# Optimization experiments

Measured on AMD Instinct MI355X. Metric: run time of the kernel, lower is better.

## Reference

```python
import jax, jax.numpy as jnp
import numpy as np

NUM_HEADS = 32
HIDDEN = 4096
HEAD_DIM = HIDDEN // NUM_HEADS
BATCH = 1
SEQ = 2048


def setup_inputs() -> dict:
    key = jax.random.key(0)
    ks = jax.random.split(key, 8)
    hidden_states = jax.random.normal(ks[0], (BATCH, SEQ, HIDDEN), dtype=jnp.float32)
    residual = jax.random.normal(ks[1], (BATCH, SEQ, HIDDEN), dtype=jnp.float32)
    # BLOOM alibi: [batch*heads, 1, kv_len], broadcast over q_length in baddbmm
    alibi = jax.random.normal(ks[2], (BATCH * NUM_HEADS, 1, SEQ), dtype=jnp.float32) * 0.1
    # causal boolean mask: True = masked (filled with -inf before softmax)
    attention_mask = ~jnp.tril(jnp.ones((SEQ, SEQ), dtype=bool))[None, None, :, :]
    scale = 0.02
    Wqkv = jax.random.normal(ks[3], (3 * HIDDEN, HIDDEN), dtype=jnp.float32) * scale
    bqkv = jax.random.normal(ks[4], (3 * HIDDEN,), dtype=jnp.float32) * scale
    Wd = jax.random.normal(ks[5], (HIDDEN, HIDDEN), dtype=jnp.float32) * scale
    bd = jax.random.normal(ks[6], (HIDDEN,), dtype=jnp.float32) * scale
    return {"hidden_states": hidden_states, "residual": residual, "alibi": alibi,
            "attention_mask": attention_mask, "Wqkv": Wqkv, "bqkv": bqkv,
            "Wd": Wd, "bd": bd}


def reference(hidden_states, residual, alibi, attention_mask, Wqkv, bqkv, Wd, bd):
    B, S, H = hidden_states.shape
    nh, hd = NUM_HEADS, HEAD_DIM
    inv_norm = 1.0 / np.sqrt(hd).astype(np.float32)

    # fused QKV projection, BLOOM interleaved layout [B, S, nh, 3, hd]
    fused = hidden_states @ Wqkv.T + bqkv           # [B, S, 3H]
    fused = fused.reshape(B, S, nh, 3, hd)
    q = jnp.transpose(fused[..., 0, :], (0, 2, 1, 3))  # [B, nh, S, hd]
    k = jnp.transpose(fused[..., 1, :], (0, 2, 1, 3))  # [B, nh, S, hd]
    v = jnp.transpose(fused[..., 2, :], (0, 2, 1, 3))  # [B, nh, S, hd]

    # baddbmm: alibi + inv_norm * Q @ K^T
    alibi_b = alibi.reshape(B, nh, 1, S)                # broadcast over q_length
    scores = alibi_b + inv_norm * jnp.einsum('bhqd,bhkd->bhqk', q, k)
    scores = jnp.where(attention_mask, jnp.finfo(scores.dtype).min, scores)
    probs = jax.nn.softmax(scores, axis=-1)             # [B, nh, S, S]

    ctx = jnp.einsum('bhqk,bhkd->bhqd', probs, v)       # [B, nh, S, hd]
    ctx = jnp.transpose(ctx, (0, 2, 1, 3)).reshape(B, S, H)
    out = ctx @ Wd.T + bd
    return residual + out
```

## Files before the change

kernel.cpp:

```cpp
#include <hip/hip_runtime.h>


#define SEQL 2048
#define HIDN 4096
#define NHEAD 32
#define HDIM 128
#define H3 12288

typedef __bf16 bf16x8 __attribute__((ext_vector_type(8)));
typedef float f32x4 __attribute__((ext_vector_type(4)));
typedef unsigned short u16x8 __attribute__((ext_vector_type(8)));

__device__ __forceinline__ unsigned short f2bf(float f) {
  union { float f; unsigned u; } v; v.f = f;
  return (unsigned short)((v.u + 0x7FFFu + ((v.u >> 16) & 1u)) >> 16);
}

__device__ __forceinline__ void gload_lds16(const void* g, void* l) {
  __builtin_amdgcn_global_load_lds(
      (const __attribute__((address_space(1))) void*)g,
      (__attribute__((address_space(3))) void*)l, 16, 0, 0);
}

__global__ __launch_bounds__(256) void cvt_f32_bf16(
    const float* __restrict__ in, unsigned short* __restrict__ out, long long n) {
  long long i = ((long long)blockIdx.x * blockDim.x + threadIdx.x) * 8;
  long long stride = (long long)gridDim.x * blockDim.x * 8;
  for (; i < n; i += stride) {
    float4 a = *(const float4*)(in + i);
    float4 b = *(const float4*)(in + i + 4);
    u16x8 o;
    o[0] = f2bf(a.x); o[1] = f2bf(a.y); o[2] = f2bf(a.z); o[3] = f2bf(a.w);
    o[4] = f2bf(b.x); o[5] = f2bf(b.y); o[6] = f2bf(b.z); o[7] = f2bf(b.w);
    *(u16x8*)(out + i) = o;
  }
}

template <int EPI>
__global__ __launch_bounds__(256) void gemm_nt(
    const unsigned short* __restrict__ A, const unsigned short* __restrict__ B,
    int M, int N, int K,
    const float* __restrict__ bias, const float* __restrict__ residual,
    float* __restrict__ outf,
    unsigned short* __restrict__ q_bf, unsigned short* __restrict__ k_bf,
    unsigned short* __restrict__ v_t) {
  __shared__ unsigned short As[128 * 64];
  __shared__ unsigned short Bs[128 * 64];

  const int tid = threadIdx.x;
  const int l = tid & 63;
  const int w = tid >> 6;
  const int wr = (w >> 1) * 64;
  const int wc = (w & 1) * 64;

  const int nb = gridDim.x;
  const int lin = (blockIdx.x & 7) * (nb >> 3) + (blockIdx.x >> 3);
  const int tm0 = (lin & 15) * 128;
  const int tn0 = (lin >> 4) * 128;

  const int lr = l >> 3;
  const int lc = (l & 7) ^ lr;

  f32x4 acc[4][4] = {};

  for (int kt = 0; kt < K; kt += 64) {
    __syncthreads();
#pragma unroll
    for (int i = 0; i < 4; ++i) {
      const int row = w * 32 + i * 8 + lr;
      gload_lds16(&A[(long long)(tm0 + row) * K + kt + lc * 8],
                  (char*)As + (w * 4 + i) * 1024);
      gload_lds16(&B[(long long)(tn0 + row) * K + kt + lc * 8],
                  (char*)Bs + (w * 4 + i) * 1024);
    }
    __syncthreads();
#pragma unroll
    for (int kk = 0; kk < 2; ++kk) {
      const int colb = kk * 64 + (l >> 4) * 16;
      bf16x8 af[4], bfr[4];
#pragma unroll
      for (int m = 0; m < 4; ++m) {
        int row = wr + m * 16 + (l & 15);
        af[m] = *(const bf16x8*)((char*)As + row * 128 + (colb ^ ((row & 7) << 4)));
      }
#pragma unroll
      for (int n = 0; n < 4; ++n) {
        int row = wc + n * 16 + (l & 15);
        bfr[n] = *(const bf16x8*)((char*)Bs + row * 128 + (colb ^ ((row & 7) << 4)));
      }
#pragma unroll
      for (int m = 0; m < 4; ++m)
#pragma unroll
        for (int n = 0; n < 4; ++n)
          acc[m][n] = __builtin_amdgcn_mfma_f32_16x16x32_bf16(af[m], bfr[n], acc[m][n], 0, 0, 0);
    }
  }

#pragma unroll
  for (int m = 0; m < 4; ++m) {
#pragma unroll
    for (int n = 0; n < 4; ++n) {
      const int col = tn0 + wc + n * 16 + (l & 15);
      const float bv = bias[col];
#pragma unroll
      for (int r = 0; r < 4; ++r) {
        const int rowg = tm0 + wr + m * 16 + (l >> 4) * 4 + r;
        float v = acc[m][n][r] + bv;
        if (EPI == 0) {
          const int head = col / 384;
          const int rem = col - head * 384;
          const int which = rem >> 7;
          const int d = rem & 127;
          const unsigned short bv16 = f2bf(v);
          if (which == 0)
            q_bf[(long long)(head * SEQL + rowg) * HDIM + d] = bv16;
          else if (which == 1)
            k_bf[(long long)(head * SEQL + rowg) * HDIM + d] = bv16;
          else
            v_t[(long long)(head * HDIM + d) * SEQL + rowg] = bv16;
        } else {
          const long long idx = (long long)rowg * N + col;
          outf[idx] = v + residual[idx];
        }
      }
    }
  }
}

__global__ __launch_bounds__(256) void attn_fwd(
    const unsigned short* __restrict__ q_bf, const unsigned short* __restrict__ k_bf,
    const unsigned short* __restrict__ v_t, const float* __restrict__ alibi,
    unsigned short* __restrict__ ctx_bf) {
  __shared__ unsigned short Ks[64 * 128];
  __shared__ unsigned short Vs[128 * 64];
  __shared__ unsigned short Ps[4][16 * 64];
  __shared__ float Al[SEQL];

  const int tid = threadIdx.x;
  const int l = tid & 63;
  const int w = tid >> 6;

  const float LOG2E = 1.4426950408889634f;

  const int b = blockIdx.x;
  const int i_ = b >> 3;
  const int h = (b & 7) * 4 + (i_ & 3);
  const int qtile = 31 - (i_ >> 2);
  const int qw = qtile * 64 + w * 16;

  for (int i = tid; i < SEQL; i += 256) Al[i] = alibi[h * SEQL + i] * LOG2E;

  bf16x8 qf[4];
  {
    const unsigned short* qp =
        &q_bf[(long long)(h * SEQL + qw + (l & 15)) * HDIM + (l >> 4) * 8];
#pragma unroll
    for (int kk = 0; kk < 4; ++kk) qf[kk] = *(const bf16x8*)(qp + kk * 32);
  }

  f32x4 oacc[8] = {};
  float mrun[4] = {-__builtin_inff(), -__builtin_inff(), -__builtin_inff(), -__builtin_inff()};
  float lrun[4] = {0.f, 0.f, 0.f, 0.f};
  const float inv_norm2 = 0.08838834764831845f * 1.4426950408889634f;

  const int kR = l >> 4, kC = l & 15;
  const int vR = l >> 3, vC = (l & 7) ^ vR;

  const int ntiles = qtile + 1;
  for (int t = 0; t < ntiles; ++t) {
    const int kv0 = t * 64;
    __syncthreads();
#pragma unroll
    for (int i = 0; i < 4; ++i) {
      const int krow = w * 16 + i * 4 + kR;
      const int ksrc = kC ^ ((i & 1) * 4 + kR);
      gload_lds16(&k_bf[(long long)(h * SEQL + kv0 + krow) * HDIM + ksrc * 8],
                  (char*)Ks + (w * 4 + i) * 1024);
      const int vrow = w * 32 + i * 8 + vR;
      gload_lds16(&v_t[(long long)(h * HDIM + vrow) * SEQL + kv0 + vC * 8],
                  (char*)Vs + (w * 4 + i) * 1024);
    }
    __syncthreads();

    f32x4 sacc[4] = {};
#pragma unroll
    for (int kk = 0; kk < 4; ++kk) {
      const int colb = kk * 64 + (l >> 4) * 16;
#pragma unroll
      for (int n = 0; n < 4; ++n) {
        int row = n * 16 + (l & 15);
        bf16x8 kf = *(const bf16x8*)((char*)Ks + row * 256 + (colb ^ ((row & 7) << 4)));
        sacc[n] = __builtin_amdgcn_mfma_f32_16x16x32_bf16(qf[kk], kf, sacc[n], 0, 0, 0);
      }
    }

    float sc[4][4];
#pragma unroll
    for (int n = 0; n < 4; ++n) {
      const int kv = kv0 + n * 16 + (l & 15);
      const float al = Al[kv];
#pragma unroll
      for (int r = 0; r < 4; ++r) {
        const int qrow = qw + (l >> 4) * 4 + r;
        float v = al + inv_norm2 * sacc[n][r];
        sc[n][r] = (kv > qrow) ? -__builtin_inff() : v;
      }
    }

#pragma unroll
    for (int r = 0; r < 4; ++r) {
      float m0 = fmaxf(fmaxf(sc[0][r], sc[1][r]), fmaxf(sc[2][r], sc[3][r]));
      m0 = fmaxf(m0, __shfl_xor(m0, 1, 64));
      m0 = fmaxf(m0, __shfl_xor(m0, 2, 64));
      m0 = fmaxf(m0, __shfl_xor(m0, 4, 64));
      m0 = fmaxf(m0, __shfl_xor(m0, 8, 64));
      if (__ballot(m0 > mrun[r] + 11.0f)) {
        const float mnew = fmaxf(mrun[r], m0);
        const float scale = exp2f(mrun[r] - mnew);
        mrun[r] = mnew;
        lrun[r] *= scale;
#pragma unroll
        for (int n2 = 0; n2 < 8; ++n2) oacc[n2][r] *= scale;
      }
      float p0 = 0.f;
#pragma unroll
      for (int n = 0; n < 4; ++n) {
        const float pv = exp2f(sc[n][r] - mrun[r]);
        sc[n][r] = pv;
        p0 += pv;
      }
      p0 += __shfl_xor(p0, 1, 64);
      p0 += __shfl_xor(p0, 2, 64);
      p0 += __shfl_xor(p0, 4, 64);
      p0 += __shfl_xor(p0, 8, 64);
      lrun[r] += p0;
    }

#pragma unroll
    for (int n = 0; n < 4; ++n)
#pragma unroll
      for (int r = 0; r < 4; ++r) {
        const int row = (l >> 4) * 4 + r;
        const int colp = n * 16 + (l & 15);
        *(unsigned short*)((char*)Ps[w] + row * 128 + ((colp * 2) ^ ((row & 7) << 4))) =
            f2bf(sc[n][r]);
      }
    __threadfence_block();
    bf16x8 pf[2];
#pragma unroll
    for (int kk2 = 0; kk2 < 2; ++kk2) {
      const int row = l & 15;
      const int colb = kk2 * 64 + (l >> 4) * 16;
      pf[kk2] = *(const bf16x8*)((char*)Ps[w] + row * 128 + (colb ^ ((row & 7) << 4)));
    }

#pragma unroll
    for (int n2 = 0; n2 < 8; ++n2) {
#pragma unroll
      for (int kk2 = 0; kk2 < 2; ++kk2) {
        const int row = n2 * 16 + (l & 15);
        const int colb = kk2 * 64 + (l >> 4) * 16;
        bf16x8 vf = *(const bf16x8*)((char*)Vs + row * 128 + (colb ^ ((row & 7) << 4)));
        oacc[n2] = __builtin_amdgcn_mfma_f32_16x16x32_bf16(pf[kk2], vf, oacc[n2], 0, 0, 0);
      }
    }
  }

#pragma unroll
  for (int n2 = 0; n2 < 8; ++n2)
#pragma unroll
    for (int r = 0; r < 4; ++r) {
      const int qrow = qw + (l >> 4) * 4 + r;
      const int col = h * HDIM + n2 * 16 + (l & 15);
      ctx_bf[(long long)qrow * HIDN + col] = f2bf(oacc[n2][r] / lrun[r]);
    }
}

extern "C" void kernel_launch(void* const* d_in, const int* in_sizes, int n_in,
                              void* d_out, int out_size, void* d_ws, size_t ws_size,
                              hipStream_t stream) {
  const float* hidden = (const float*)d_in[0];
  const float* residual = (const float*)d_in[1];
  const float* alibi = (const float*)d_in[2];
  const float* Wqkv = (const float*)d_in[4];
  const float* bqkv = (const float*)d_in[5];
  const float* Wd = (const float*)d_in[6];
  const float* bd = (const float*)d_in[7];
  float* out = (float*)d_out;

  char* ws = (char*)d_ws;
  const size_t MB16 = 16777216;
  unsigned short* q_bf = (unsigned short*)(ws);
  unsigned short* k_bf = (unsigned short*)(ws + MB16);
  unsigned short* v_t = (unsigned short*)(ws + 2 * MB16);
  unsigned short* hid_bf = (unsigned short*)(ws + 3 * MB16);
  unsigned short* wqkv_bf = (unsigned short*)(ws + 4 * MB16);
  unsigned short* wd_bf = (unsigned short*)(ws + 4 * MB16);
  unsigned short* ctx_bf = (unsigned short*)(ws + 4 * MB16 + 33554432);

  cvt_f32_bf16<<<4096, 256, 0, stream>>>(hidden, hid_bf, (long long)SEQL * HIDN);
  cvt_f32_bf16<<<24576, 256, 0, stream>>>(Wqkv, wqkv_bf, (long long)H3 * HIDN);

  gemm_nt<0><<<(SEQL / 128) * (H3 / 128), 256, 0, stream>>>(
      hid_bf, wqkv_bf, SEQL, H3, HIDN, bqkv, nullptr, nullptr, q_bf, k_bf, v_t);

  cvt_f32_bf16<<<8192, 256, 0, stream>>>(Wd, wd_bf, (long long)HIDN * HIDN);

  attn_fwd<<<NHEAD * (SEQL / 64), 256, 0, stream>>>(q_bf, k_bf, v_t, alibi, ctx_bf);

  gemm_nt<1><<<(SEQL / 128) * (HIDN / 128), 256, 0, stream>>>(
      ctx_bf, wd_bf, SEQL, HIDN, HIDN, bd, residual, out, nullptr, nullptr, nullptr);
}
```

Baseline: 503.4 us.

## Double-buffer K/V tiles in attention with async prefetch and wave-level causal skip

The attention kernel now double-buffers K and V tiles in LDS. The next tile is issued with global_load_lds before computing the current one, and explicit vmcnt waits plus raw barriers replace the two __syncthreads per iteration. Waves whose 16 query rows lie entirely before the KV tile skip the score/softmax/PV work, and the alibi preload is limited to the needed length. This doubles K/V LDS use (about 64KB plus alibi), which may reduce occupancy, and relies on hand-counted vmcnt values being correct.

```diff
diff --git a/kernel.cpp b/kernel.cpp
--- a/kernel.cpp
+++ b/kernel.cpp
@@ -21,6 +21,14 @@
       (const __attribute__((address_space(1))) void*)g,
       (__attribute__((address_space(3))) void*)l, 16, 0, 0);
 }
+
+#define BARX()                                  \
+  do {                                          \
+    __builtin_amdgcn_sched_barrier(0);          \
+    __builtin_amdgcn_s_barrier();               \
+    __builtin_amdgcn_sched_barrier(0);          \
+  } while (0)
+#define VMW(n) asm volatile("s_waitcnt vmcnt(" #n ")" ::: "memory")
 
 __global__ __launch_bounds__(256) void cvt_f32_bf16(
     const float* __restrict__ in, unsigned short* __restrict__ out, long long n) {
@@ -131,8 +139,8 @@
     const unsigned short* __restrict__ q_bf, const unsigned short* __restrict__ k_bf,
     const unsigned short* __restrict__ v_t, const float* __restrict__ alibi,
     unsigned short* __restrict__ ctx_bf) {
-  __shared__ unsigned short Ks[64 * 128];
-  __shared__ unsigned short Vs[128 * 64];
+  __shared__ unsigned short Ks[2][64 * 128];
+  __shared__ unsigned short Vs[2][128 * 64];
   __shared__ unsigned short Ps[4][16 * 64];
   __shared__ float Al[SEQL];
 
@@ -147,8 +155,11 @@
   const int h = (b & 7) * 4 + (i_ & 3);
   const int qtile = 31 - (i_ >> 2);
   const int qw = qtile * 64 + w * 16;
-
-  for (int i = tid; i < SEQL; i += 256) Al[i] = alibi[h * SEQL + i] * LOG2E;
+  const int ntiles = qtile + 1;
+
+  const int alN = ntiles * 64;
+  for (int i = tid; i < alN; i += 256) Al[i] = alibi[h * SEQL + i] * LOG2E;
+  asm volatile("s_waitcnt lgkmcnt(0)" ::: "memory");
 
   bf16x8 qf[4];
   {
@@ -166,104 +177,118 @@
   const int kR = l >> 4, kC = l & 15;
   const int vR = l >> 3, vC = (l & 7) ^ vR;
 
-  const int ntiles = qtile + 1;
-  for (int t = 0; t < ntiles; ++t) {
+  auto stage = [&](int t) {
+    const int buf = t & 1;
     const int kv0 = t * 64;
-    __syncthreads();
 #pragma unroll
     for (int i = 0; i < 4; ++i) {
-      const int krow = w * 16 + i * 4 + kR;
+      const int c = w * 4 + i;
+      const int krow = c * 4 + kR;
       const int ksrc = kC ^ ((i & 1) * 4 + kR);
       gload_lds16(&k_bf[(long long)(h * SEQL + kv0 + krow) * HDIM + ksrc * 8],
-                  (char*)Ks + (w * 4 + i) * 1024);
-      const int vrow = w * 32 + i * 8 + vR;
+                  (char*)Ks[buf] + c * 1024);
+      const int vrow = c * 8 + vR;
       gload_lds16(&v_t[(long long)(h * HDIM + vrow) * SEQL + kv0 + vC * 8],
-                  (char*)Vs + (w * 4 + i) * 1024);
-    }
-    __syncthreads();
-
-    f32x4 sacc[4] = {};
-#pragma unroll
-    for (int kk = 0; kk < 4; ++kk) {
-      const int colb = kk * 64 + (l >> 4) * 16;
+                  (char*)Vs[buf] + c * 1024);
+    }
+  };
+
+  stage(0);
+  for (int t = 0; t < ntiles; ++t) {
+    const int cur = t & 1;
+    const int kv0 = t * 64;
+    const bool g = (t + 1) < ntiles;
+    if (g) stage(t + 1);
+    if (g) { VMW(8); } else { VMW(0); }
+    BARX();
+
+    if (kv0 <= qw + 15) {
+      f32x4 sacc[4] = {};
+#pragma unroll
+      for (int kk = 0; kk < 4; ++kk) {
+        const int colb = kk * 64 + (l >> 4) * 16;
+#pragma unroll
+        for (int n = 0; n < 4; ++n) {
+          int row = n * 16 + (l & 15);
+          bf16x8 kf = *(const bf16x8*)((char*)Ks[cur] + row * 256 +
+                                       (colb ^ ((row & 7) << 4)));
+          sacc[n] = __builtin_amdgcn_mfma_f32_16x16x32_bf16(qf[kk], kf, sacc[n], 0, 0, 0);
+        }
+      }
+
+      float sc[4][4];
 #pragma unroll
       for (int n = 0; n < 4; ++n) {
-        int row = n * 16 + (l & 15);
-        bf16x8 kf = *(const bf16x8*)((char*)Ks + row * 256 + (colb ^ ((row & 7) << 4)));
-        sacc[n] = __builtin_amdgcn_mfma_f32_16x16x32_bf16(qf[kk], kf, sacc[n], 0, 0, 0);
-      }
-    }
-
-    float sc[4][4];
-#pragma unroll
-    for (int n = 0; n < 4; ++n) {
-      const int kv = kv0 + n * 16 + (l & 15);
-      const float al = Al[kv];
+        const int kv = kv0 + n * 16 + (l & 15);
+        const float al = Al[kv];
+#pragma unroll
+        for (int r = 0; r < 4; ++r) {
+          const int qrow = qw + (l >> 4) * 4 + r;
+          float v = al + inv_norm2 * sacc[n][r];
+          sc[n][r] = (kv > qrow) ? -__builtin_inff() : v;
+        }
+      }
+
 #pragma unroll
       for (int r = 0; r < 4; ++r) {
-        const int qrow = qw + (l >> 4) * 4 + r;
-        float v = al + inv_norm2 * sacc[n][r];
-        sc[n][r] = (kv > qrow) ? -__builtin_inff() : v;
-      }
-    }
-
-#pragma unroll
-    for (int r = 0; r < 4; ++r) {
-      float m0 = fmaxf(fmaxf(sc[0][r], sc[1][r]), fmaxf(sc[2][r], sc[3][r]));
-      m0 = fmaxf(m0, __shfl_xor(m0, 1, 64));
-      m0 = fmaxf(m0, __shfl_xor(m0, 2, 64));
-      m0 = fmaxf(m0, __shfl_xor(m0, 4, 64));
-      m0 = fmaxf(m0, __shfl_xor(m0, 8, 64));
-      if (__ballot(m0 > mrun[r] + 11.0f)) {
-        const float mnew = fmaxf(mrun[r], m0);
-        const float scale = exp2f(mrun[r] - mnew);
-        mrun[r] = mnew;
-        lrun[r] *= scale;
-#pragma unroll
-        for (int n2 = 0; n2 < 8; ++n2) oacc[n2][r] *= scale;
-      }
-      float p0 = 0.f;
-#pragma unroll
-      for (int n = 0; n < 4; ++n) {
-        const float pv = exp2f(sc[n][r] - mrun[r]);
-        sc[n][r] = pv;
-        p0 += pv;
-      }
-      p0 += __shfl_xor(p0, 1, 64);
-      p0 += __shfl_xor(p0, 2, 64);
-      p0 += __shfl_xor(p0, 4, 64);
-      p0 += __shfl_xor(p0, 8, 64);
-      lrun[r] += p0;
-    }
-
-#pragma unroll
-    for (int n = 0; n < 4; ++n)
-#pragma unroll
-      for (int r = 0; r < 4; ++r) {
-        const int row = (l >> 4) * 4 + r;
-        const int colp = n * 16 + (l & 15);
-        *(unsigned short*)((char*)Ps[w] + row * 128 + ((colp * 2) ^ ((row & 7) << 4))) =
-            f2bf(sc[n][r]);
-      }
-    __threadfence_block();
-    bf16x8 pf[2];
-#pragma unroll
-    for (int kk2 = 0; kk2 < 2; ++kk2) {
-      const int row = l & 15;
-      const int colb = kk2 * 64 + (l >> 4) * 16;
-      pf[kk2] = *(const bf16x8*)((char*)Ps[w] + row * 128 + (colb ^ ((row & 7) << 4)));
-    }
-
-#pragma unroll
-    for (int n2 = 0; n2 < 8; ++n2) {
+        float m0 = fmaxf(fmaxf(sc[0][r], sc[1][r]), fmaxf(sc[2][r], sc[3][r]));
+        m0 = fmaxf(m0, __shfl_xor(m0, 1, 64));
+        m0 = fmaxf(m0, __shfl_xor(m0, 2, 64));
+        m0 = fmaxf(m0, __shfl_xor(m0, 4, 64));
+        m0 = fmaxf(m0, __shfl_xor(m0, 8, 64));
+        if (__ballot(m0 > mrun[r] + 11.0f)) {
+          const float mnew = fmaxf(mrun[r], m0);
+          const float scale = exp2f(mrun[r] - mnew);
+          mrun[r] = mnew;
+          lrun[r] *= scale;
+#pragma unroll
+          for (int n2 = 0; n2 < 8; ++n2) oacc[n2][r] *= scale;
+        }
+        float p0 = 0.f;
+#pragma unroll
+        for (int n = 0; n < 4; ++n) {
+          const float pv = exp2f(sc[n][r] - mrun[r]);
+          sc[n][r] = pv;
+          p0 += pv;
+        }
+        p0 += __shfl_xor(p0, 1, 64);
+        p0 += __shfl_xor(p0, 2, 64);
+        p0 += __shfl_xor(p0, 4, 64);
+        p0 += __shfl_xor(p0, 8, 64);
+        lrun[r] += p0;
+      }
+
+#pragma unroll
+      for (int n = 0; n < 4; ++n)
+#pragma unroll
+        for (int r = 0; r < 4; ++r) {
+          const int row = (l >> 4) * 4 + r;
+          const int colp = n * 16 + (l & 15);
+          *(unsigned short*)((char*)Ps[w] + row * 128 + ((colp * 2) ^ ((row & 7) << 4))) =
+              f2bf(sc[n][r]);
+        }
+      __threadfence_block();
+      bf16x8 pf[2];
 #pragma unroll
       for (int kk2 = 0; kk2 < 2; ++kk2) {
-        const int row = n2 * 16 + (l & 15);
+        const int row = l & 15;
         const int colb = kk2 * 64 + (l >> 4) * 16;
-        bf16x8 vf = *(const bf16x8*)((char*)Vs + row * 128 + (colb ^ ((row & 7) << 4)));
-        oacc[n2] = __builtin_amdgcn_mfma_f32_16x16x32_bf16(pf[kk2], vf, oacc[n2], 0, 0, 0);
-      }
-    }
+        pf[kk2] = *(const bf16x8*)((char*)Ps[w] + row * 128 + (colb ^ ((row & 7) << 4)));
+      }
+
+#pragma unroll
+      for (int n2 = 0; n2 < 8; ++n2) {
+#pragma unroll
+        for (int kk2 = 0; kk2 < 2; ++kk2) {
+          const int row = n2 * 16 + (l & 15);
+          const int colb = kk2 * 64 + (l >> 4) * 16;
+          bf16x8 vf = *(const bf16x8*)((char*)Vs[cur] + row * 128 +
+                                       (colb ^ ((row & 7) << 4)));
+          oacc[n2] = __builtin_amdgcn_mfma_f32_16x16x32_bf16(pf[kk2], vf, oacc[n2], 0, 0, 0);
+        }
+      }
+    }
+    BARX();
   }
 
 #pragma unroll
```

Measured after the change: 506.8 us. About the same (+0.7%).

## Process 128 query rows per attention block, two 16-row groups per wave

Applied to the files above, without the earlier changes.

The attention kernel now gives each block a 128-row query tile, with each wave handling 32 rows as two 16-row MFMA groups. Each K/V tile loaded into LDS is reused across twice as many queries, which halves global K/V traffic and the per-tile barrier overhead. Waves skip KV tiles that lie fully above their causal diagonal. The cost is more registers for the doubled accumulators, and there are half as many blocks (512), which may lower occupancy and load balance across CUs.

```diff
diff --git a/kernel.cpp b/kernel.cpp
--- a/kernel.cpp
+++ b/kernel.cpp
@@ -133,7 +133,7 @@
     unsigned short* __restrict__ ctx_bf) {
   __shared__ unsigned short Ks[64 * 128];
   __shared__ unsigned short Vs[128 * 64];
-  __shared__ unsigned short Ps[4][16 * 64];
+  __shared__ unsigned short Ps[4][32 * 64];
   __shared__ float Al[SEQL];
 
   const int tid = threadIdx.x;
@@ -145,135 +145,154 @@
   const int b = blockIdx.x;
   const int i_ = b >> 3;
   const int h = (b & 7) * 4 + (i_ & 3);
-  const int qtile = 31 - (i_ >> 2);
-  const int qw = qtile * 64 + w * 16;
-
-  for (int i = tid; i < SEQL; i += 256) Al[i] = alibi[h * SEQL + i] * LOG2E;
-
-  bf16x8 qf[4];
-  {
+  const int qtile = 15 - (i_ >> 2);
+  const int qw = qtile * 128 + w * 32;
+  const int ntiles = 2 * qtile + 2;
+
+  for (int i = tid; i < ntiles * 64; i += 256) Al[i] = alibi[h * SEQL + i] * LOG2E;
+
+  bf16x8 qf[2][4];
+#pragma unroll
+  for (int g = 0; g < 2; ++g) {
     const unsigned short* qp =
-        &q_bf[(long long)(h * SEQL + qw + (l & 15)) * HDIM + (l >> 4) * 8];
-#pragma unroll
-    for (int kk = 0; kk < 4; ++kk) qf[kk] = *(const bf16x8*)(qp + kk * 32);
-  }
-
-  f32x4 oacc[8] = {};
-  float mrun[4] = {-__builtin_inff(), -__builtin_inff(), -__builtin_inff(), -__builtin_inff()};
-  float lrun[4] = {0.f, 0.f, 0.f, 0.f};
+        &q_bf[(long long)(h * SEQL + qw + g * 16 + (l & 15)) * HDIM + (l >> 4) * 8];
+#pragma unroll
+    for (int kk = 0; kk < 4; ++kk) qf[g][kk] = *(const bf16x8*)(qp + kk * 32);
+  }
+
+  f32x4 oacc[2][8] = {};
+  float mrun[2][4], lrun[2][4];
+#pragma unroll
+  for (int g = 0; g < 2; ++g)
+#pragma unroll
+    for (int r = 0; r < 4; ++r) { mrun[g][r] = -__builtin_inff(); lrun[g][r] = 0.f; }
   const float inv_norm2 = 0.08838834764831845f * 1.4426950408889634f;
 
   const int kR = l >> 4, kC = l & 15;
   const int vR = l >> 3, vC = (l & 7) ^ vR;
 
-  const int ntiles = qtile + 1;
   for (int t = 0; t < ntiles; ++t) {
     const int kv0 = t * 64;
     __syncthreads();
 #pragma unroll
     for (int i = 0; i < 4; ++i) {
-      const int krow = w * 16 + i * 4 + kR;
+      const int c = w * 4 + i;
+      const int krow = c * 4 + kR;
       const int ksrc = kC ^ ((i & 1) * 4 + kR);
       gload_lds16(&k_bf[(long long)(h * SEQL + kv0 + krow) * HDIM + ksrc * 8],
-                  (char*)Ks + (w * 4 + i) * 1024);
-      const int vrow = w * 32 + i * 8 + vR;
+                  (char*)Ks + c * 1024);
+      const int vrow = c * 8 + vR;
       gload_lds16(&v_t[(long long)(h * HDIM + vrow) * SEQL + kv0 + vC * 8],
-                  (char*)Vs + (w * 4 + i) * 1024);
+                  (char*)Vs + c * 1024);
     }
     __syncthreads();
 
-    f32x4 sacc[4] = {};
-#pragma unroll
-    for (int kk = 0; kk < 4; ++kk) {
-      const int colb = kk * 64 + (l >> 4) * 16;
-#pragma unroll
-      for (int n = 0; n < 4; ++n) {
-        int row = n * 16 + (l & 15);
-        bf16x8 kf = *(const bf16x8*)((char*)Ks + row * 256 + (colb ^ ((row & 7) << 4)));
-        sacc[n] = __builtin_amdgcn_mfma_f32_16x16x32_bf16(qf[kk], kf, sacc[n], 0, 0, 0);
-      }
-    }
-
-    float sc[4][4];
-#pragma unroll
-    for (int n = 0; n < 4; ++n) {
-      const int kv = kv0 + n * 16 + (l & 15);
-      const float al = Al[kv];
+    if (kv0 <= qw + 31) {
+      f32x4 sacc[2][4] = {};
+#pragma unroll
+      for (int kk = 0; kk < 4; ++kk) {
+        const int colb = kk * 64 + (l >> 4) * 16;
+#pragma unroll
+        for (int n = 0; n < 4; ++n) {
+          const int row = n * 16 + (l & 15);
+          bf16x8 kf = *(const bf16x8*)((char*)Ks + row * 256 +
+                                       (colb ^ ((row & 7) << 4)));
+          sacc[0][n] = __builtin_amdgcn_mfma_f32_16x16x32_bf16(qf[0][kk], kf, sacc[0][n], 0, 0, 0);
+          sacc[1][n] = __builtin_amdgcn_mfma_f32_16x16x32_bf16(qf[1][kk], kf, sacc[1][n], 0, 0, 0);
+        }
+      }
+
+#pragma unroll
+      for (int g = 0; g < 2; ++g) {
+        const int qwg = qw + g * 16;
+        float sc[4][4];
+#pragma unroll
+        for (int n = 0; n < 4; ++n) {
+          const int kv = kv0 + n * 16 + (l & 15);
+          const float al = Al[kv];
+#pragma unroll
+          for (int r = 0; r < 4; ++r) {
+            const int qrow = qwg + (l >> 4) * 4 + r;
+            float v = al + inv_norm2 * sacc[g][n][r];
+            sc[n][r] = (kv > qrow) ? -__builtin_inff() : v;
+          }
+        }
+#pragma unroll
+        for (int r = 0; r < 4; ++r) {
+          float m0 = fmaxf(fmaxf(sc[0][r], sc[1][r]), fmaxf(sc[2][r], sc[3][r]));
+          m0 = fmaxf(m0, __shfl_xor(m0, 1, 64));
+          m0 = fmaxf(m0, __shfl_xor(m0, 2, 64));
+          m0 = fmaxf(m0, __shfl_xor(m0, 4, 64));
+          m0 = fmaxf(m0, __shfl_xor(m0, 8, 64));
+          if (__ballot(m0 > mrun[g][r] + 11.0f)) {
+            const float mnew = fmaxf(mrun[g][r], m0);
+            const float scale = exp2f(mrun[g][r] - mnew);
+            mrun[g][r] = mnew;
+            lrun[g][r] *= scale;
+#pragma unroll
+            for (int n2 = 0; n2 < 8; ++n2) oacc[g][n2][r] *= scale;
+          }
+          float p0 = 0.f;
+#pragma unroll
+          for (int n = 0; n < 4; ++n) {
+            const float pv = exp2f(sc[n][r] - mrun[g][r]);
+            sc[n][r] = pv;
+            p0 += pv;
+          }
+          p0 += __shfl_xor(p0, 1, 64);
+          p0 += __shfl_xor(p0, 2, 64);
+          p0 += __shfl_xor(p0, 4, 64);
+          p0 += __shfl_xor(p0, 8, 64);
+          lrun[g][r] += p0;
+        }
+#pragma unroll
+        for (int n = 0; n < 4; ++n)
+#pragma unroll
+          for (int r = 0; r < 4; ++r) {
+            const int row = g * 16 + (l >> 4) * 4 + r;
+            const int colp = n * 16 + (l & 15);
+            *(unsigned short*)((char*)Ps[w] + row * 128 +
+                               ((colp * 2) ^ ((row & 7) << 4))) = f2bf(sc[n][r]);
+          }
+      }
+      __threadfence_block();
+
+      bf16x8 pf[2][2];
+#pragma unroll
+      for (int g = 0; g < 2; ++g)
+#pragma unroll
+        for (int kk2 = 0; kk2 < 2; ++kk2) {
+          const int row = g * 16 + (l & 15);
+          const int colb = kk2 * 64 + (l >> 4) * 16;
+          pf[g][kk2] = *(const bf16x8*)((char*)Ps[w] + row * 128 +
+                                        (colb ^ ((row & 7) << 4)));
+        }
+
+#pragma unroll
+      for (int n2 = 0; n2 < 8; ++n2) {
+#pragma unroll
+        for (int kk2 = 0; kk2 < 2; ++kk2) {
+          const int row = n2 * 16 + (l & 15);
+          const int colb = kk2 * 64 + (l >> 4) * 16;
+          bf16x8 vf = *(const bf16x8*)((char*)Vs + row * 128 +
+                                       (colb ^ ((row & 7) << 4)));
+          oacc[0][n2] = __builtin_amdgcn_mfma_f32_16x16x32_bf16(pf[0][kk2], vf, oacc[0][n2], 0, 0, 0);
+          oacc[1][n2] = __builtin_amdgcn_mfma_f32_16x16x32_bf16(pf[1][kk2], vf, oacc[1][n2], 0, 0, 0);
+        }
+      }
+    }
+  }
+
+#pragma unroll
+  for (int g = 0; g < 2; ++g)
+#pragma unroll
+    for (int n2 = 0; n2 < 8; ++n2)
 #pragma unroll
       for (int r = 0; r < 4; ++r) {
-        const int qrow = qw + (l >> 4) * 4 + r;
-        float v = al + inv_norm2 * sacc[n][r];
-        sc[n][r] = (kv > qrow) ? -__builtin_inff() : v;
-      }
-    }
-
-#pragma unroll
-    for (int r = 0; r < 4; ++r) {
-      float m0 = fmaxf(fmaxf(sc[0][r], sc[1][r]), fmaxf(sc[2][r], sc[3][r]));
-      m0 = fmaxf(m0, __shfl_xor(m0, 1, 64));
-      m0 = fmaxf(m0, __shfl_xor(m0, 2, 64));
-      m0 = fmaxf(m0, __shfl_xor(m0, 4, 64));
-      m0 = fmaxf(m0, __shfl_xor(m0, 8, 64));
-      if (__ballot(m0 > mrun[r] + 11.0f)) {
-        const float mnew = fmaxf(mrun[r], m0);
-        const float scale = exp2f(mrun[r] - mnew);
-        mrun[r] = mnew;
-        lrun[r] *= scale;
-#pragma unroll
-        for (int n2 = 0; n2 < 8; ++n2) oacc[n2][r] *= scale;
-      }
-      float p0 = 0.f;
-#pragma unroll
-      for (int n = 0; n < 4; ++n) {
-        const float pv = exp2f(sc[n][r] - mrun[r]);
-        sc[n][r] = pv;
-        p0 += pv;
-      }
-      p0 += __shfl_xor(p0, 1, 64);
-      p0 += __shfl_xor(p0, 2, 64);
-      p0 += __shfl_xor(p0, 4, 64);
-      p0 += __shfl_xor(p0, 8, 64);
-      lrun[r] += p0;
-    }
-
-#pragma unroll
-    for (int n = 0; n < 4; ++n)
-#pragma unroll
-      for (int r = 0; r < 4; ++r) {
-        const int row = (l >> 4) * 4 + r;
-        const int colp = n * 16 + (l & 15);
-        *(unsigned short*)((char*)Ps[w] + row * 128 + ((colp * 2) ^ ((row & 7) << 4))) =
-            f2bf(sc[n][r]);
-      }
-    __threadfence_block();
-    bf16x8 pf[2];
-#pragma unroll
-    for (int kk2 = 0; kk2 < 2; ++kk2) {
-      const int row = l & 15;
-      const int colb = kk2 * 64 + (l >> 4) * 16;
-      pf[kk2] = *(const bf16x8*)((char*)Ps[w] + row * 128 + (colb ^ ((row & 7) << 4)));
-    }
-
-#pragma unroll
-    for (int n2 = 0; n2 < 8; ++n2) {
-#pragma unroll
-      for (int kk2 = 0; kk2 < 2; ++kk2) {
-        const int row = n2 * 16 + (l & 15);
-        const int colb = kk2 * 64 + (l >> 4) * 16;
-        bf16x8 vf = *(const bf16x8*)((char*)Vs + row * 128 + (colb ^ ((row & 7) << 4)));
-        oacc[n2] = __builtin_amdgcn_mfma_f32_16x16x32_bf16(pf[kk2], vf, oacc[n2], 0, 0, 0);
-      }
-    }
-  }
-
-#pragma unroll
-  for (int n2 = 0; n2 < 8; ++n2)
-#pragma unroll
-    for (int r = 0; r < 4; ++r) {
-      const int qrow = qw + (l >> 4) * 4 + r;
-      const int col = h * HDIM + n2 * 16 + (l & 15);
-      ctx_bf[(long long)qrow * HIDN + col] = f2bf(oacc[n2][r] / lrun[r]);
-    }
+        const int qrow = qw + g * 16 + (l >> 4) * 4 + r;
+        const int col = h * HDIM + n2 * 16 + (l & 15);
+        ctx_bf[(long long)qrow * HIDN + col] = f2bf(oacc[g][n2][r] / lrun[g][r]);
+      }
 }
 
 extern "C" void kernel_launch(void* const* d_in, const int* in_sizes, int n_in,
@@ -306,7 +325,7 @@
 
   cvt_f32_bf16<<<8192, 256, 0, stream>>>(Wd, wd_bf, (long long)HIDN * HIDN);
 
-  attn_fwd<<<NHEAD * (SEQL / 64), 256, 0, stream>>>(q_bf, k_bf, v_t, alibi, ctx_bf);
+  attn_fwd<<<NHEAD * (SEQL / 128), 256, 0, stream>>>(q_bf, k_bf, v_t, alibi, ctx_bf);
 
   gemm_nt<1><<<(SEQL / 128) * (HIDN / 128), 256, 0, stream>>>(
       ctx_bf, wd_bf, SEQL, HIDN, HIDN, bd, residual, out, nullptr, nullptr, nullptr);
```

Result: slower. 538.4 us (+7.0%).

## Transpose attention MFMA operands to keep P in registers and vectorize output

Applied to the files above, without the earlier changes.

Swaps the MFMA operand order so each lane holds one query row's scores. The row max and sum then need only two cross-lane shuffles, and mrun and lrun become scalars. P is packed into bf16 with v_cvt_pk_bf16_f32 and redistributed by register shuffles instead of a round trip through shared memory. Each warp also skips KV tiles that lie fully above its causal diagonal, and the context output is staged through shared memory so it can be written with 16-byte stores. The costs are extra shuffle and select work and a divergent branch around the per-warp tile skip, while the block-wide syncs remain.

```diff
diff --git a/kernel.cpp b/kernel.cpp
--- a/kernel.cpp
+++ b/kernel.cpp
@@ -10,10 +10,17 @@
 typedef __bf16 bf16x8 __attribute__((ext_vector_type(8)));
 typedef float f32x4 __attribute__((ext_vector_type(4)));
 typedef unsigned short u16x8 __attribute__((ext_vector_type(8)));
+typedef unsigned int u32x4 __attribute__((ext_vector_type(4)));
 
 __device__ __forceinline__ unsigned short f2bf(float f) {
   union { float f; unsigned u; } v; v.f = f;
   return (unsigned short)((v.u + 0x7FFFu + ((v.u >> 16) & 1u)) >> 16);
+}
+
+__device__ __forceinline__ unsigned cvtpk(float lo, float hi) {
+  unsigned r;
+  asm("v_cvt_pk_bf16_f32 %0, %1, %2" : "=v"(r) : "v"(lo), "v"(hi));
+  return r;
 }
 
 __device__ __forceinline__ void gload_lds16(const void* g, void* l) {
@@ -133,12 +140,13 @@
     unsigned short* __restrict__ ctx_bf) {
   __shared__ unsigned short Ks[64 * 128];
   __shared__ unsigned short Vs[128 * 64];
-  __shared__ unsigned short Ps[4][16 * 64];
   __shared__ float Al[SEQL];
 
   const int tid = threadIdx.x;
   const int l = tid & 63;
   const int w = tid >> 6;
+  const int q = l & 15;
+  const int g = l >> 4;
 
   const float LOG2E = 1.4426950408889634f;
 
@@ -147,26 +155,27 @@
   const int h = (b & 7) * 4 + (i_ & 3);
   const int qtile = 31 - (i_ >> 2);
   const int qw = qtile * 64 + w * 16;
+  const int qrow = qw + q;
+  const int ntiles = qtile + 1;
 
   for (int i = tid; i < SEQL; i += 256) Al[i] = alibi[h * SEQL + i] * LOG2E;
 
   bf16x8 qf[4];
   {
     const unsigned short* qp =
-        &q_bf[(long long)(h * SEQL + qw + (l & 15)) * HDIM + (l >> 4) * 8];
+        &q_bf[(long long)(h * SEQL + qw + q) * HDIM + g * 8];
 #pragma unroll
     for (int kk = 0; kk < 4; ++kk) qf[kk] = *(const bf16x8*)(qp + kk * 32);
   }
 
   f32x4 oacc[8] = {};
-  float mrun[4] = {-__builtin_inff(), -__builtin_inff(), -__builtin_inff(), -__builtin_inff()};
-  float lrun[4] = {0.f, 0.f, 0.f, 0.f};
+  float mrun = -__builtin_inff();
+  float lrun = 0.f;
   const float inv_norm2 = 0.08838834764831845f * 1.4426950408889634f;
 
   const int kR = l >> 4, kC = l & 15;
   const int vR = l >> 3, vC = (l & 7) ^ vR;
 
-  const int ntiles = qtile + 1;
   for (int t = 0; t < ntiles; ++t) {
     const int kv0 = t * 64;
     __syncthreads();
@@ -182,98 +191,113 @@
     }
     __syncthreads();
 
-    f32x4 sacc[4] = {};
-#pragma unroll
-    for (int kk = 0; kk < 4; ++kk) {
-      const int colb = kk * 64 + (l >> 4) * 16;
+    if (kv0 <= qw + 15) {
+      f32x4 sacc[4] = {};
+#pragma unroll
+      for (int kk = 0; kk < 4; ++kk) {
+        const int colb = kk * 64 + g * 16;
+#pragma unroll
+        for (int n = 0; n < 4; ++n) {
+          const int row = n * 16 + q;
+          bf16x8 kf = *(const bf16x8*)((char*)Ks + row * 256 + (colb ^ ((row & 7) << 4)));
+          sacc[n] = __builtin_amdgcn_mfma_f32_16x16x32_bf16(kf, qf[kk], sacc[n], 0, 0, 0);
+        }
+      }
+
+      float p[4][4];
+      float m0 = -__builtin_inff();
 #pragma unroll
       for (int n = 0; n < 4; ++n) {
-        int row = n * 16 + (l & 15);
-        bf16x8 kf = *(const bf16x8*)((char*)Ks + row * 256 + (colb ^ ((row & 7) << 4)));
-        sacc[n] = __builtin_amdgcn_mfma_f32_16x16x32_bf16(qf[kk], kf, sacc[n], 0, 0, 0);
-      }
-    }
-
-    float sc[4][4];
-#pragma unroll
-    for (int n = 0; n < 4; ++n) {
-      const int kv = kv0 + n * 16 + (l & 15);
-      const float al = Al[kv];
+        const f32x4 alv = *(const f32x4*)(Al + kv0 + n * 16 + g * 4);
+#pragma unroll
+        for (int r = 0; r < 4; ++r) {
+          const int kv = kv0 + n * 16 + g * 4 + r;
+          float v = alv[r] + inv_norm2 * sacc[n][r];
+          v = (kv > qrow) ? -__builtin_inff() : v;
+          p[n][r] = v;
+          m0 = fmaxf(m0, v);
+        }
+      }
+      m0 = fmaxf(m0, __shfl_xor(m0, 16, 64));
+      m0 = fmaxf(m0, __shfl_xor(m0, 32, 64));
+      if (__ballot(m0 > mrun + 11.0f)) {
+        const float mnew = fmaxf(mrun, m0);
+        const float scale = exp2f(mrun - mnew);
+        mrun = mnew;
+        lrun *= scale;
+#pragma unroll
+        for (int n2 = 0; n2 < 8; ++n2)
+#pragma unroll
+          for (int r = 0; r < 4; ++r) oacc[n2][r] *= scale;
+      }
+      float p0 = 0.f;
+#pragma unroll
+      for (int n = 0; n < 4; ++n)
+#pragma unroll
+        for (int r = 0; r < 4; ++r) {
+          const float pv = exp2f(p[n][r] - mrun);
+          p[n][r] = pv;
+          p0 += pv;
+        }
+      p0 += __shfl_xor(p0, 16, 64);
+      p0 += __shfl_xor(p0, 32, 64);
+      lrun += p0;
+
+      bf16x8 pb[2];
+#pragma unroll
+      for (int kk2 = 0; kk2 < 2; ++kk2) {
+        const int n0 = 2 * kk2;
+        const unsigned pk0 = cvtpk(p[n0][0], p[n0][1]);
+        const unsigned pk1 = cvtpk(p[n0][2], p[n0][3]);
+        const unsigned pk2 = cvtpk(p[n0 + 1][0], p[n0 + 1][1]);
+        const unsigned pk3 = cvtpk(p[n0 + 1][2], p[n0 + 1][3]);
+        const int s0 = q + 32 * (g & 1);
+        const int s2 = s0 + 16;
+        const unsigned a0 = __shfl((int)pk0, s0, 64), b0 = __shfl((int)pk2, s0, 64);
+        const unsigned a1 = __shfl((int)pk1, s0, 64), b1 = __shfl((int)pk3, s0, 64);
+        const unsigned a2 = __shfl((int)pk0, s2, 64), b2 = __shfl((int)pk2, s2, 64);
+        const unsigned a3 = __shfl((int)pk1, s2, 64), b3 = __shfl((int)pk3, s2, 64);
+        const bool lo = (g < 2);
+        u32x4 wv;
+        wv[0] = lo ? a0 : b0; wv[1] = lo ? a1 : b1;
+        wv[2] = lo ? a2 : b2; wv[3] = lo ? a3 : b3;
+        pb[kk2] = __builtin_bit_cast(bf16x8, wv);
+      }
+
+#pragma unroll
+      for (int n2 = 0; n2 < 8; ++n2) {
+#pragma unroll
+        for (int kk2 = 0; kk2 < 2; ++kk2) {
+          const int row = n2 * 16 + q;
+          const int colb = kk2 * 64 + g * 16;
+          bf16x8 vf = *(const bf16x8*)((char*)Vs + row * 128 + (colb ^ ((row & 7) << 4)));
+          oacc[n2] = __builtin_amdgcn_mfma_f32_16x16x32_bf16(vf, pb[kk2], oacc[n2], 0, 0, 0);
+        }
+      }
+    }
+  }
+
+  __syncthreads();
+  {
+    char* scr = (char*)Ks + w * 4096;
+    const float rdiv = 1.0f / lrun;
+#pragma unroll
+    for (int n2 = 0; n2 < 8; ++n2)
 #pragma unroll
       for (int r = 0; r < 4; ++r) {
-        const int qrow = qw + (l >> 4) * 4 + r;
-        float v = al + inv_norm2 * sacc[n][r];
-        sc[n][r] = (kv > qrow) ? -__builtin_inff() : v;
-      }
-    }
-
-#pragma unroll
-    for (int r = 0; r < 4; ++r) {
-      float m0 = fmaxf(fmaxf(sc[0][r], sc[1][r]), fmaxf(sc[2][r], sc[3][r]));
-      m0 = fmaxf(m0, __shfl_xor(m0, 1, 64));
-      m0 = fmaxf(m0, __shfl_xor(m0, 2, 64));
-      m0 = fmaxf(m0, __shfl_xor(m0, 4, 64));
-      m0 = fmaxf(m0, __shfl_xor(m0, 8, 64));
-      if (__ballot(m0 > mrun[r] + 11.0f)) {
-        const float mnew = fmaxf(mrun[r], m0);
-        const float scale = exp2f(mrun[r] - mnew);
-        mrun[r] = mnew;
-        lrun[r] *= scale;
-#pragma unroll
-        for (int n2 = 0; n2 < 8; ++n2) oacc[n2][r] *= scale;
-      }
-      float p0 = 0.f;
-#pragma unroll
-      for (int n = 0; n < 4; ++n) {
-        const float pv = exp2f(sc[n][r] - mrun[r]);
-        sc[n][r] = pv;
-        p0 += pv;
-      }
-      p0 += __shfl_xor(p0, 1, 64);
-      p0 += __shfl_xor(p0, 2, 64);
-      p0 += __shfl_xor(p0, 4, 64);
-      p0 += __shfl_xor(p0, 8, 64);
-      lrun[r] += p0;
-    }
-
-#pragma unroll
-    for (int n = 0; n < 4; ++n)
-#pragma unroll
-      for (int r = 0; r < 4; ++r) {
-        const int row = (l >> 4) * 4 + r;
-        const int colp = n * 16 + (l & 15);
-        *(unsigned short*)((char*)Ps[w] + row * 128 + ((colp * 2) ^ ((row & 7) << 4))) =
-            f2bf(sc[n][r]);
+        const int d = n2 * 16 + g * 4 + r;
+        *(unsigned short*)(scr + ((q * 256 + d * 2) ^ ((q & 7) << 4))) =
+            f2bf(oacc[n2][r] * rdiv);
       }
     __threadfence_block();
-    bf16x8 pf[2];
-#pragma unroll
-    for (int kk2 = 0; kk2 < 2; ++kk2) {
-      const int row = l & 15;
-      const int colb = kk2 * 64 + (l >> 4) * 16;
-      pf[kk2] = *(const bf16x8*)((char*)Ps[w] + row * 128 + (colb ^ ((row & 7) << 4)));
-    }
-
-#pragma unroll
-    for (int n2 = 0; n2 < 8; ++n2) {
-#pragma unroll
-      for (int kk2 = 0; kk2 < 2; ++kk2) {
-        const int row = n2 * 16 + (l & 15);
-        const int colb = kk2 * 64 + (l >> 4) * 16;
-        bf16x8 vf = *(const bf16x8*)((char*)Vs + row * 128 + (colb ^ ((row & 7) << 4)));
-        oacc[n2] = __builtin_amdgcn_mfma_f32_16x16x32_bf16(pf[kk2], vf, oacc[n2], 0, 0, 0);
-      }
-    }
-  }
-
-#pragma unroll
-  for (int n2 = 0; n2 < 8; ++n2)
-#pragma unroll
-    for (int r = 0; r < 4; ++r) {
-      const int qrow = qw + (l >> 4) * 4 + r;
-      const int col = h * HDIM + n2 * 16 + (l & 15);
-      ctx_bf[(long long)qrow * HIDN + col] = f2bf(oacc[n2][r] / lrun[r]);
-    }
+    const int q2 = l >> 2;
+#pragma unroll
+    for (int i = 0; i < 4; ++i) {
+      const int chunk = (l & 3) + i * 4;
+      u16x8 v = *(const u16x8*)(scr + ((q2 * 256 + chunk * 16) ^ ((q2 & 7) << 4)));
+      *(u16x8*)&ctx_bf[(long long)(qw + q2) * HIDN + h * HDIM + chunk * 8] = v;
+    }
+  }
 }
 
 extern "C" void kernel_launch(void* const* d_in, const int* in_sizes, int n_in,
```

Result: faster. 475.8 us (median of 2 runs) (-5.5%).
